# Kernel optimization log

Hardware: AMD Instinct MI355X
Metric: run time of the kernel (lower is better)

The kernel has to match this reference:

```python
import jax, jax.numpy as jnp
import numpy as np

B, S, D = 4, 2048, 1024
H, HK = 16, 4          # num_heads, num_heads_kv
HD = D // H            # head_dim = 64
G = H // HK            # kv groups = 4


def setup_inputs() -> dict:
    key = jax.random.key(0)
    ks = jax.random.split(key, 7)
    s = 0.02
    return {
        "query": jax.random.normal(ks[0], (B, S, D), jnp.float32),
        "key":   jax.random.normal(ks[1], (B, S, D), jnp.float32),
        "value": jax.random.normal(ks[2], (B, S, D), jnp.float32),
        # weights stored (in, out); equivalent to torch Linear y = x @ W.T
        "Wq": jax.random.normal(ks[3], (D, H * HD), jnp.float32) * s,
        "Wk": jax.random.normal(ks[4], (D, HK * HD), jnp.float32) * s,
        "Wv": jax.random.normal(ks[5], (D, HK * HD), jnp.float32) * s,
        "Wo": jax.random.normal(ks[6], (H * HD, D), jnp.float32) * s,
    }


def reference(query, key, value, Wq, Wk, Wv, Wo):
    b, qlen, _ = query.shape
    kvlen = key.shape[1]
    # projections
    q = (query @ Wq).reshape(b, qlen, H, HD)        # [b,q,H,hd]
    k = (key @ Wk).reshape(b, kvlen, HK, HD)        # [b,s,HK,hd]
    v = (value @ Wv).reshape(b, kvlen, HK, HD)      # [b,s,HK,hd]
    # GQA: q head h attends kv head h//G (repeat_interleave semantics)
    qg = q.reshape(b, qlen, HK, G, HD)              # head = kv*G + group
    scale = 1.0 / jnp.sqrt(jnp.asarray(HD, q.dtype))
    # scores [b,HK,G,q,s] -- broadcast kv heads, no materialized repeat
    scores = jnp.einsum('bqkgd,bskd->bkgqs', qg, k) * scale
    attn = jax.nn.softmax(scores, axis=-1)
    out = jnp.einsum('bkgqs,bskd->bqkgd', attn, v)  # [b,q,HK,G,hd]
    out = out.reshape(b, qlen, H * HD)
    return out @ Wo
```

## Files before the change

kernel.cpp:

```cpp
#include <hip/hip_runtime.h>


typedef unsigned short u16;
typedef unsigned int   u32;
typedef __bf16 bf16x4 __attribute__((ext_vector_type(4)));
typedef __bf16 bf16x8 __attribute__((ext_vector_type(8)));
typedef float  f32x4  __attribute__((ext_vector_type(4)));

#define MFMA(a,b,c) __builtin_amdgcn_mfma_f32_16x16x32_bf16((a),(b),(c),0,0,0)

__device__ __forceinline__ u16 f2bf(float f){
    u32 u = __builtin_bit_cast(u32, f);
    u += 0x7fffu + ((u >> 16) & 1u);
    return (u16)(u >> 16);
}
__device__ __forceinline__ bf16x8 ldfrag(const u16* p){
    return *(const bf16x8*)p;
}
__device__ __forceinline__ bf16x8 ld2x64(const u16* p){
    bf16x4 lo = *(const bf16x4*)p;
    bf16x4 hi = *(const bf16x4*)(p + 4);
    bf16x8 r;
    r[0]=lo[0]; r[1]=lo[1]; r[2]=lo[2]; r[3]=lo[3];
    r[4]=hi[0]; r[5]=hi[1]; r[6]=hi[2]; r[7]=hi[3];
    return r;
}

__device__ __forceinline__ void wcast_body(const float* __restrict__ W,
                                           u16* __restrict__ WT, int K, int N){
    __shared__ float T[32][33];
    int kt = blockIdx.x * 32, nt = blockIdx.y * 32;
    if (nt >= N) return;
    int r = threadIdx.x >> 3, c = threadIdx.x & 7;
    float4 v = *(const float4*)(W + (size_t)(kt + r) * N + nt + c * 4);
    T[r][c*4+0] = v.x; T[r][c*4+1] = v.y; T[r][c*4+2] = v.z; T[r][c*4+3] = v.w;
    __syncthreads();
    u32 lo = (u32)f2bf(T[c*4+0][r]) | ((u32)f2bf(T[c*4+1][r]) << 16);
    u32 hi = (u32)f2bf(T[c*4+2][r]) | ((u32)f2bf(T[c*4+3][r]) << 16);
    *(uint2*)(WT + (size_t)(nt + r) * K + kt + c * 4) = make_uint2(lo, hi);
}
__global__ __launch_bounds__(256) void wcast4(const float* W0, const float* W1,
                                              const float* W2, const float* W3,
                                              u16* T0, u16* T1, u16* T2, u16* T3){
    switch (blockIdx.z){
        case 0: wcast_body(W0, T0, 1024, 1024); break;
        case 1: wcast_body(W1, T1, 1024,  256); break;
        case 2: wcast_body(W2, T2, 1024,  256); break;
        default: wcast_body(W3, T3, 1024, 1024); break;
    }
}

template<int ATYPE, int EPI>
__device__ __forceinline__ void gemm_body(const void* __restrict__ Ap,
                                          const u16* __restrict__ Bt,
                                          void* __restrict__ Cp,
                                          int N, int K, int m0, int n0,
                                          u16* As, u16* Bs){
    const int tid  = threadIdx.x;
    const int wave = tid >> 6, lane = tid & 63;
    const int quad = lane >> 4, l15 = lane & 15;
    const int wm = wave >> 1, wn = wave & 1;

    f32x4 acc[4][4];
    #pragma unroll
    for (int i = 0; i < 4; ++i)
        #pragma unroll
        for (int j = 0; j < 4; ++j) acc[i][j] = (f32x4){0.f, 0.f, 0.f, 0.f};

    const int nkt = K >> 6;
    for (int kt = 0; kt < nkt; ++kt){
        __syncthreads();
        if constexpr (ATYPE == 0){
            const float* A = (const float*)Ap;
            int c4 = tid & 15, r0 = tid >> 4;
            #pragma unroll
            for (int p = 0; p < 8; ++p){
                int r = r0 + p * 16;
                float4 v = *(const float4*)(A + (size_t)(m0 + r) * K + kt * 64 + c4 * 4);
                u32 lo = (u32)f2bf(v.x) | ((u32)f2bf(v.y) << 16);
                u32 hi = (u32)f2bf(v.z) | ((u32)f2bf(v.w) << 16);
                *(uint2*)&As[r * 80 + c4 * 4] = make_uint2(lo, hi);
            }
        } else {
            const u16* A = (const u16*)Ap;
            int c8 = tid & 7, r0 = tid >> 3;
            #pragma unroll
            for (int p = 0; p < 4; ++p){
                int r = r0 + p * 32;
                *(uint4*)&As[r * 80 + c8 * 8] =
                    *(const uint4*)(A + (size_t)(m0 + r) * K + kt * 64 + c8 * 8);
            }
        }
        {
            int c8 = tid & 7, r0 = tid >> 3;
            #pragma unroll
            for (int p = 0; p < 4; ++p){
                int r = r0 + p * 32;
                *(uint4*)&Bs[r * 80 + c8 * 8] =
                    *(const uint4*)(Bt + (size_t)(n0 + r) * K + kt * 64 + c8 * 8);
            }
        }
        __syncthreads();
        #pragma unroll
        for (int ks = 0; ks < 2; ++ks){
            bf16x8 af[4], bfr[4];
            #pragma unroll
            for (int mt = 0; mt < 4; ++mt)
                af[mt] = ldfrag(&As[(wm*64 + mt*16 + l15) * 80 + ks*32 + quad*8]);
            #pragma unroll
            for (int nt = 0; nt < 4; ++nt)
                bfr[nt] = ldfrag(&Bs[(wn*64 + nt*16 + l15) * 80 + ks*32 + quad*8]);
            #pragma unroll
            for (int mt = 0; mt < 4; ++mt)
                #pragma unroll
                for (int nt = 0; nt < 4; ++nt)
                    acc[mt][nt] = MFMA(af[mt], bfr[nt], acc[mt][nt]);
        }
    }
    #pragma unroll
    for (int mt = 0; mt < 4; ++mt){
        int rowb = m0 + wm*64 + mt*16 + quad*4;
        #pragma unroll
        for (int nt = 0; nt < 4; ++nt){
            int col = n0 + wn*64 + nt*16 + l15;
            if constexpr (EPI == 0){
                u16* C = (u16*)Cp;
                #pragma unroll
                for (int r = 0; r < 4; ++r)
                    C[(size_t)(rowb + r) * N + col] = f2bf(acc[mt][nt][r]);
            } else if constexpr (EPI == 2){
                float* C = (float*)Cp;
                #pragma unroll
                for (int r = 0; r < 4; ++r)
                    C[(size_t)(rowb + r) * N + col] = acc[mt][nt][r];
            } else {
                u16* C = (u16*)Cp;
                int bb = rowb >> 11, s = rowb & 2047;
                u32 lo = (u32)f2bf(acc[mt][nt][0]) | ((u32)f2bf(acc[mt][nt][1]) << 16);
                u32 hi = (u32)f2bf(acc[mt][nt][2]) | ((u32)f2bf(acc[mt][nt][3]) << 16);
                *(uint2*)(C + (size_t)(bb * 256 + col) * 2048 + s) = make_uint2(lo, hi);
            }
        }
    }
}

template<int ATYPE, int EPI>
__global__ __launch_bounds__(256) void gemm_k(const void* __restrict__ Ap,
                                              const u16* __restrict__ Bt,
                                              void* __restrict__ Cp,
                                              int N, int K){
    __shared__ u16 As[128 * 80];
    __shared__ u16 Bs[128 * 80];
    gemm_body<ATYPE, EPI>(Ap, Bt, Cp, N, K, blockIdx.y * 128, blockIdx.x * 128, As, Bs);
}

__global__ __launch_bounds__(256) void gemm_kv(const void* __restrict__ key,
                                               const u16* __restrict__ WkT,
                                               void* __restrict__ Kp,
                                               const void* __restrict__ value,
                                               const u16* __restrict__ WvT,
                                               void* __restrict__ Vt){
    __shared__ u16 As[128 * 80];
    __shared__ u16 Bs[128 * 80];
    if (blockIdx.z == 0)
        gemm_body<0,0>(key,   WkT, Kp, 256, 1024, blockIdx.y * 128, blockIdx.x * 128, As, Bs);
    else
        gemm_body<0,1>(value, WvT, Vt, 256, 1024, blockIdx.y * 128, blockIdx.x * 128, As, Bs);
}

__global__ __launch_bounds__(256, 4) void attn_k(const u16* __restrict__ Qp,
                                                 const u16* __restrict__ Kp,
                                                 const u16* __restrict__ Vt,
                                                 u16* __restrict__ AO){
    constexpr int S = 2048, Dm = 1024, NKV = 256, HD = 64;
    __shared__ u16 Ks[64 * 72];
    __shared__ u16 Vs[64 * 72];
    __shared__ u16 Ps[4 * 32 * 68];
    const int tid = threadIdx.x, wave = tid >> 6, lane = tid & 63;
    const int quad = lane >> 4, l15 = lane & 15;
    const int qt = blockIdx.x, h = blockIdx.y, b = blockIdx.z;
    const int hk = h >> 2, q0 = qt * 128;
    u16* pw = Ps + wave * (32 * 68);

    {
        int c8 = tid & 7, r0 = tid >> 3;
        #pragma unroll
        for (int p = 0; p < 4; ++p){
            int r = r0 + p * 32;
            uint4 v = *(const uint4*)(Qp + (size_t)(b * S + q0 + r) * Dm + h * HD + c8 * 8);
            *(uint2*)&Ps[r * 68 + c8 * 8]     = make_uint2(v.x, v.y);
            *(uint2*)&Ps[r * 68 + c8 * 8 + 4] = make_uint2(v.z, v.w);
        }
    }
    __syncthreads();
    bf16x8 qf[2][2];
    #pragma unroll
    for (int mt = 0; mt < 2; ++mt)
        #pragma unroll
        for (int ks = 0; ks < 2; ++ks)
            qf[mt][ks] = ld2x64(&Ps[(wave*32 + mt*16 + l15) * 68 + ks*32 + quad*8]);

    f32x4 O[2][4];
    #pragma unroll
    for (int mt = 0; mt < 2; ++mt)
        #pragma unroll
        for (int nt = 0; nt < 4; ++nt) O[mt][nt] = (f32x4){0.f, 0.f, 0.f, 0.f};
    float psum[2][4];
    #pragma unroll
    for (int mt = 0; mt < 2; ++mt)
        #pragma unroll
        for (int r = 0; r < 4; ++r) psum[mt][r] = 0.f;
    const float cexp = 0.125f * 1.44269504f;

    for (int t = 0; t < 32; ++t){
        int j0 = t * 64;
        __syncthreads();
        {
            int c8 = tid & 7, r0 = tid >> 3;
            #pragma unroll
            for (int p = 0; p < 2; ++p){
                int r = r0 + p * 32;
                *(uint4*)&Ks[r * 72 + c8 * 8] =
                    *(const uint4*)(Kp + (size_t)(b * S + j0 + r) * NKV + hk * HD + c8 * 8);
                *(uint4*)&Vs[r * 72 + c8 * 8] =
                    *(const uint4*)(Vt + (size_t)(b * NKV + hk * HD + r) * S + j0 + c8 * 8);
            }
        }
        __syncthreads();
        f32x4 sf[2][4];
        #pragma unroll
        for (int mt = 0; mt < 2; ++mt)
            #pragma unroll
            for (int nt = 0; nt < 4; ++nt) sf[mt][nt] = (f32x4){0.f, 0.f, 0.f, 0.f};
        #pragma unroll
        for (int ks = 0; ks < 2; ++ks){
            #pragma unroll
            for (int nt = 0; nt < 4; ++nt){
                bf16x8 bk = ldfrag(&Ks[(nt*16 + l15) * 72 + ks*32 + quad*8]);
                #pragma unroll
                for (int mt = 0; mt < 2; ++mt)
                    sf[mt][nt] = MFMA(qf[mt][ks], bk, sf[mt][nt]);
            }
        }
        #pragma unroll
        for (int mt = 0; mt < 2; ++mt)
            #pragma unroll
            for (int nt = 0; nt < 4; ++nt)
                #pragma unroll
                for (int r = 0; r < 4; ++r){
                    float e = exp2f(sf[mt][nt][r] * cexp);
                    psum[mt][r] += e;
                    pw[(mt*16 + quad*4 + r) * 68 + nt*16 + l15] = f2bf(e);
                }
        __threadfence_block();
        #pragma unroll
        for (int ks = 0; ks < 2; ++ks){
            bf16x8 ap[2];
            #pragma unroll
            for (int mt = 0; mt < 2; ++mt)
                ap[mt] = ld2x64(&pw[(mt*16 + l15) * 68 + ks*32 + quad*8]);
            #pragma unroll
            for (int nt = 0; nt < 4; ++nt){
                bf16x8 bv = ldfrag(&Vs[(nt*16 + l15) * 72 + ks*32 + quad*8]);
                #pragma unroll
                for (int mt = 0; mt < 2; ++mt)
                    O[mt][nt] = MFMA(ap[mt], bv, O[mt][nt]);
            }
        }
    }
    #pragma unroll
    for (int mt = 0; mt < 2; ++mt)
        #pragma unroll
        for (int r = 0; r < 4; ++r){
            float v = psum[mt][r];
            v += __shfl_xor(v, 1); v += __shfl_xor(v, 2);
            v += __shfl_xor(v, 4); v += __shfl_xor(v, 8);
            psum[mt][r] = 1.0f / v;
        }
    #pragma unroll
    for (int mt = 0; mt < 2; ++mt)
        #pragma unroll
        for (int r = 0; r < 4; ++r){
            int row = b * S + q0 + wave*32 + mt*16 + quad*4 + r;
            #pragma unroll
            for (int nt = 0; nt < 4; ++nt)
                AO[(size_t)row * Dm + h * HD + nt*16 + l15] =
                    f2bf(O[mt][nt][r] * psum[mt][r]);
        }
}

extern "C" void kernel_launch(void* const* d_in, const int* in_sizes, int n_in,
                              void* d_out, int out_size, void* d_ws, size_t ws_size,
                              hipStream_t stream){
    const float* q  = (const float*)d_in[0];
    const float* k  = (const float*)d_in[1];
    const float* v  = (const float*)d_in[2];
    const float* Wq = (const float*)d_in[3];
    const float* Wk = (const float*)d_in[4];
    const float* Wv = (const float*)d_in[5];
    const float* Wo = (const float*)d_in[6];
    char* ws = (char*)d_ws;
    u16* WqT = (u16*)(ws);
    u16* WkT = (u16*)(ws + (size_t)(2u  << 20));
    u16* WvT = (u16*)(ws + (size_t)(2560u << 10));
    u16* WoT = (u16*)(ws + (size_t)(3u  << 20));
    u16* Qp  = (u16*)(ws + (size_t)(5u  << 20));
    u16* Kp  = (u16*)(ws + (size_t)(21u << 20));
    u16* Vt  = (u16*)(ws + (size_t)(25u << 20));
    u16* AO  = (u16*)(ws + (size_t)(29u << 20));

    wcast4<<<dim3(32, 32, 4), 256, 0, stream>>>(Wq, Wk, Wv, Wo, WqT, WkT, WvT, WoT);

    gemm_k<0,0><<<dim3(8, 64), 256, 0, stream>>>((const void*)q, WqT, (void*)Qp, 1024, 1024);
    gemm_kv<<<dim3(2, 64, 2), 256, 0, stream>>>((const void*)k, WkT, (void*)Kp,
                                                (const void*)v, WvT, (void*)Vt);

    attn_k<<<dim3(16, 16, 4), 256, 0, stream>>>(Qp, Kp, Vt, AO);

    gemm_k<1,2><<<dim3(8, 64), 256, 0, stream>>>((const void*)AO, WoT, d_out, 1024, 1024);
}
```

Measured before the change: 353.3 us.

## Use direct global-to-LDS loads, packed bf16 converts, fold softmax scale into Q

The bf16 operand tiles of the GEMMs are now loaded with global_load_lds straight into unpadded 64-wide LDS rows, skipping the round trip through registers. Software bf16 rounding is replaced by the hardware packed convert when the builtin is available. The softmax scale times log2(e) is folded into the Q projection epilogue, which removes a multiply per score in the attention loop. Unpadded LDS rows may add bank conflicts on fragment reads, and pre-scaling Q before bf16 rounding slightly changes numerics.

```diff
diff --git a/kernel.cpp b/kernel.cpp
--- a/kernel.cpp
+++ b/kernel.cpp
@@ -9,11 +9,25 @@
 
 #define MFMA(a,b,c) __builtin_amdgcn_mfma_f32_16x16x32_bf16((a),(b),(c),0,0,0)
 
+#define GLDS(g, l) __builtin_amdgcn_global_load_lds(                          \
+    (const __attribute__((address_space(1))) void*)(g),                       \
+    (__attribute__((address_space(3))) void*)(l), 16, 0, 0)
+
 __device__ __forceinline__ u16 f2bf(float f){
     u32 u = __builtin_bit_cast(u32, f);
     u += 0x7fffu + ((u >> 16) & 1u);
     return (u16)(u >> 16);
 }
+__device__ __forceinline__ u32 pk2(float a, float b){
+#if __has_builtin(__builtin_amdgcn_cvt_pk_bf16_f32)
+    auto r = __builtin_amdgcn_cvt_pk_bf16_f32(a, b);
+    return __builtin_bit_cast(u32, r);
+#else
+    return (u32)f2bf(a) | ((u32)f2bf(b) << 16);
+#endif
+}
+__device__ __forceinline__ u16 cvt1(float a){ return (u16)pk2(a, 0.f); }
+
 __device__ __forceinline__ bf16x8 ldfrag(const u16* p){
     return *(const bf16x8*)p;
 }
@@ -35,8 +49,8 @@
     float4 v = *(const float4*)(W + (size_t)(kt + r) * N + nt + c * 4);
     T[r][c*4+0] = v.x; T[r][c*4+1] = v.y; T[r][c*4+2] = v.z; T[r][c*4+3] = v.w;
     __syncthreads();
-    u32 lo = (u32)f2bf(T[c*4+0][r]) | ((u32)f2bf(T[c*4+1][r]) << 16);
-    u32 hi = (u32)f2bf(T[c*4+2][r]) | ((u32)f2bf(T[c*4+3][r]) << 16);
+    u32 lo = pk2(T[c*4+0][r], T[c*4+1][r]);
+    u32 hi = pk2(T[c*4+2][r], T[c*4+3][r]);
     *(uint2*)(WT + (size_t)(nt + r) * K + kt + c * 4) = make_uint2(lo, hi);
 }
 __global__ __launch_bounds__(256) void wcast4(const float* W0, const float* W1,
@@ -55,7 +69,8 @@
                                           const u16* __restrict__ Bt,
                                           void* __restrict__ Cp,
                                           int N, int K, int m0, int n0,
-                                          u16* As, u16* Bs){
+                                          u16* As, u16* Bs, float oscale){
+    constexpr int ASTR = (ATYPE == 0) ? 80 : 64;
     const int tid  = threadIdx.x;
     const int wave = tid >> 6, lane = tid & 63;
     const int quad = lane >> 4, l15 = lane & 15;
@@ -77,28 +92,22 @@
             for (int p = 0; p < 8; ++p){
                 int r = r0 + p * 16;
                 float4 v = *(const float4*)(A + (size_t)(m0 + r) * K + kt * 64 + c4 * 4);
-                u32 lo = (u32)f2bf(v.x) | ((u32)f2bf(v.y) << 16);
-                u32 hi = (u32)f2bf(v.z) | ((u32)f2bf(v.w) << 16);
-                *(uint2*)&As[r * 80 + c4 * 4] = make_uint2(lo, hi);
+                *(uint2*)&As[r * 80 + c4 * 4] = make_uint2(pk2(v.x, v.y), pk2(v.z, v.w));
             }
         } else {
             const u16* A = (const u16*)Ap;
-            int c8 = tid & 7, r0 = tid >> 3;
-            #pragma unroll
-            for (int p = 0; p < 4; ++p){
-                int r = r0 + p * 32;
-                *(uint4*)&As[r * 80 + c8 * 8] =
-                    *(const uint4*)(A + (size_t)(m0 + r) * K + kt * 64 + c8 * 8);
-            }
+            const u16* ga = A + (size_t)(m0 + wave*32 + (lane>>3)) * K + kt*64 + (lane&7)*8;
+            u16* la = As + (wave*32) * 64;
+            #pragma unroll
+            for (int p = 0; p < 4; ++p)
+                GLDS(ga + (size_t)(p*8) * K, la + p*8*64);
         }
         {
-            int c8 = tid & 7, r0 = tid >> 3;
-            #pragma unroll
-            for (int p = 0; p < 4; ++p){
-                int r = r0 + p * 32;
-                *(uint4*)&Bs[r * 80 + c8 * 8] =
-                    *(const uint4*)(Bt + (size_t)(n0 + r) * K + kt * 64 + c8 * 8);
-            }
+            const u16* gb = Bt + (size_t)(n0 + wave*32 + (lane>>3)) * K + kt*64 + (lane&7)*8;
+            u16* lb = Bs + (wave*32) * 64;
+            #pragma unroll
+            for (int p = 0; p < 4; ++p)
+                GLDS(gb + (size_t)(p*8) * K, lb + p*8*64);
         }
         __syncthreads();
         #pragma unroll
@@ -106,10 +115,10 @@
             bf16x8 af[4], bfr[4];
             #pragma unroll
             for (int mt = 0; mt < 4; ++mt)
-                af[mt] = ldfrag(&As[(wm*64 + mt*16 + l15) * 80 + ks*32 + quad*8]);
+                af[mt] = ldfrag(&As[(wm*64 + mt*16 + l15) * ASTR + ks*32 + quad*8]);
             #pragma unroll
             for (int nt = 0; nt < 4; ++nt)
-                bfr[nt] = ldfrag(&Bs[(wn*64 + nt*16 + l15) * 80 + ks*32 + quad*8]);
+                bfr[nt] = ldfrag(&Bs[(wn*64 + nt*16 + l15) * 64 + ks*32 + quad*8]);
             #pragma unroll
             for (int mt = 0; mt < 4; ++mt)
                 #pragma unroll
@@ -127,7 +136,7 @@
                 u16* C = (u16*)Cp;
                 #pragma unroll
                 for (int r = 0; r < 4; ++r)
-                    C[(size_t)(rowb + r) * N + col] = f2bf(acc[mt][nt][r]);
+                    C[(size_t)(rowb + r) * N + col] = cvt1(acc[mt][nt][r] * oscale);
             } else if constexpr (EPI == 2){
                 float* C = (float*)Cp;
                 #pragma unroll
@@ -136,8 +145,8 @@
             } else {
                 u16* C = (u16*)Cp;
                 int bb = rowb >> 11, s = rowb & 2047;
-                u32 lo = (u32)f2bf(acc[mt][nt][0]) | ((u32)f2bf(acc[mt][nt][1]) << 16);
-                u32 hi = (u32)f2bf(acc[mt][nt][2]) | ((u32)f2bf(acc[mt][nt][3]) << 16);
+                u32 lo = pk2(acc[mt][nt][0], acc[mt][nt][1]);
+                u32 hi = pk2(acc[mt][nt][2], acc[mt][nt][3]);
                 *(uint2*)(C + (size_t)(bb * 256 + col) * 2048 + s) = make_uint2(lo, hi);
             }
         }
@@ -148,10 +157,11 @@
 __global__ __launch_bounds__(256) void gemm_k(const void* __restrict__ Ap,
                                               const u16* __restrict__ Bt,
                                               void* __restrict__ Cp,
-                                              int N, int K){
-    __shared__ u16 As[128 * 80];
-    __shared__ u16 Bs[128 * 80];
-    gemm_body<ATYPE, EPI>(Ap, Bt, Cp, N, K, blockIdx.y * 128, blockIdx.x * 128, As, Bs);
+                                              int N, int K, float oscale){
+    __shared__ u16 As[128 * ((ATYPE == 0) ? 80 : 64)];
+    __shared__ u16 Bs[128 * 64];
+    gemm_body<ATYPE, EPI>(Ap, Bt, Cp, N, K, blockIdx.y * 128, blockIdx.x * 128,
+                          As, Bs, oscale);
 }
 
 __global__ __launch_bounds__(256) void gemm_kv(const void* __restrict__ key,
@@ -161,11 +171,13 @@
                                                const u16* __restrict__ WvT,
                                                void* __restrict__ Vt){
     __shared__ u16 As[128 * 80];
-    __shared__ u16 Bs[128 * 80];
+    __shared__ u16 Bs[128 * 64];
     if (blockIdx.z == 0)
-        gemm_body<0,0>(key,   WkT, Kp, 256, 1024, blockIdx.y * 128, blockIdx.x * 128, As, Bs);
+        gemm_body<0,0>(key,   WkT, Kp, 256, 1024, blockIdx.y * 128, blockIdx.x * 128,
+                       As, Bs, 1.0f);
     else
-        gemm_body<0,1>(value, WvT, Vt, 256, 1024, blockIdx.y * 128, blockIdx.x * 128, As, Bs);
+        gemm_body<0,1>(value, WvT, Vt, 256, 1024, blockIdx.y * 128, blockIdx.x * 128,
+                       As, Bs, 1.0f);
 }
 
 __global__ __launch_bounds__(256, 4) void attn_k(const u16* __restrict__ Qp,
@@ -210,7 +222,6 @@
     for (int mt = 0; mt < 2; ++mt)
         #pragma unroll
         for (int r = 0; r < 4; ++r) psum[mt][r] = 0.f;
-    const float cexp = 0.125f * 1.44269504f;
 
     for (int t = 0; t < 32; ++t){
         int j0 = t * 64;
@@ -248,9 +259,9 @@
             for (int nt = 0; nt < 4; ++nt)
                 #pragma unroll
                 for (int r = 0; r < 4; ++r){
-                    float e = exp2f(sf[mt][nt][r] * cexp);
+                    float e = exp2f(sf[mt][nt][r]);
                     psum[mt][r] += e;
-                    pw[(mt*16 + quad*4 + r) * 68 + nt*16 + l15] = f2bf(e);
+                    pw[(mt*16 + quad*4 + r) * 68 + nt*16 + l15] = cvt1(e);
                 }
         __threadfence_block();
         #pragma unroll
@@ -285,7 +296,7 @@
             #pragma unroll
             for (int nt = 0; nt < 4; ++nt)
                 AO[(size_t)row * Dm + h * HD + nt*16 + l15] =
-                    f2bf(O[mt][nt][r] * psum[mt][r]);
+                    cvt1(O[mt][nt][r] * psum[mt][r]);
         }
 }
 
@@ -309,13 +320,17 @@
     u16* Vt  = (u16*)(ws + (size_t)(25u << 20));
     u16* AO  = (u16*)(ws + (size_t)(29u << 20));
 
+    const float cexp = 0.125f * 1.44269504f;
+
     wcast4<<<dim3(32, 32, 4), 256, 0, stream>>>(Wq, Wk, Wv, Wo, WqT, WkT, WvT, WoT);
 
-    gemm_k<0,0><<<dim3(8, 64), 256, 0, stream>>>((const void*)q, WqT, (void*)Qp, 1024, 1024);
+    gemm_k<0,0><<<dim3(8, 64), 256, 0, stream>>>((const void*)q, WqT, (void*)Qp,
+                                                 1024, 1024, cexp);
     gemm_kv<<<dim3(2, 64, 2), 256, 0, stream>>>((const void*)k, WkT, (void*)Kp,
                                                 (const void*)v, WvT, (void*)Vt);
 
     attn_k<<<dim3(16, 16, 4), 256, 0, stream>>>(Qp, Kp, Vt, AO);
 
-    gemm_k<1,2><<<dim3(8, 64), 256, 0, stream>>>((const void*)AO, WoT, d_out, 1024, 1024);
-}
+    gemm_k<1,2><<<dim3(8, 64), 256, 0, stream>>>((const void*)AO, WoT, d_out,
+                                                 1024, 1024, 1.0f);
+}
```

Measured after the change: 351.2 us. About the same (-0.6%).
